# Performance work log

Measured on AMD Instinct MI355X. Metric: run time of the kernel, lower is better.

The kernel has to match this reference:

```python
import jax, jax.numpy as jnp
from jax import lax
import numpy as np

DIM = 512      # latent channel dim
K = 1024       # codebook size
KS = 320       # conv kernel size (== stride -> non-overlapping frames)
STRIDE = 320
B, L = 16, 160000  # 10s of 16kHz audio


def setup_inputs() -> dict:
    key = jax.random.key(0)
    ks = jax.random.split(key, 8)
    wav = jax.random.normal(ks[0], (B, 1, L), jnp.float32)
    enc_w = jax.random.normal(ks[1], (DIM, 1, KS), jnp.float32) * 0.05
    enc_b = jnp.zeros((DIM,), jnp.float32)
    codebook = jax.random.normal(ks[2], (K, DIM), jnp.float32)
    lin_w = jax.random.normal(ks[3], (DIM, DIM), jnp.float32) * 0.02
    lin_b = jnp.zeros((DIM,), jnp.float32)
    film_w = jax.random.normal(ks[4], (2 * DIM, DIM), jnp.float32) * 0.02
    film_b = jnp.zeros((2 * DIM,), jnp.float32)
    dec_w = jax.random.normal(ks[5], (DIM, 1, KS), jnp.float32) * 0.05
    dec_b = jnp.zeros((1,), jnp.float32)
    return dict(wav=wav, enc_w=enc_w, enc_b=enc_b, codebook=codebook,
                lin_w=lin_w, lin_b=lin_b, film_w=film_w, film_b=film_b,
                dec_w=dec_w, dec_b=dec_b)


def reference(wav, enc_w, enc_b, codebook, lin_w, lin_b, film_w, film_b, dec_w, dec_b):
    # --- NAC encoder: strided Conv1d, wav [B,1,L] -> emb [B,D,T] ---
    emb = lax.conv_general_dilated(
        wav, enc_w, window_strides=(STRIDE,), padding='VALID',
        dimension_numbers=('NCH', 'OIH', 'NCH')) + enc_b[None, :, None]

    # --- time-averaged embedding for conditioning ---
    time_avg = emb.mean(axis=-1)  # [B, D]

    # --- VQ encode: nearest codebook entry per frame ---
    x = emb.transpose(0, 2, 1)  # [B, T, D]
    # squared L2 distances [B, T, K]
    dist = (x * x).sum(-1, keepdims=True) \
         - 2.0 * jnp.einsum('btd,kd->btk', x, codebook) \
         + (codebook * codebook).sum(-1)
    codes = jnp.argmin(dist, axis=-1)  # [B, T] int

    # --- VQ decode: codebook gather ---
    emb_r = codebook[codes].transpose(0, 2, 1)  # [B, D, T]

    # --- linear on pooled embedding ---
    cond = time_avg @ lin_w.T + lin_b  # [B, D]

    # --- FiLM modulation: gamma * x + beta per channel ---
    gb = cond @ film_w.T + film_b      # [B, 2D]
    gamma, beta = jnp.split(gb, 2, axis=-1)
    modulated = gamma[:, :, None] * emb_r + beta[:, :, None]  # [B, D, T]

    # --- NAC decoder: transposed Conv1d back to waveform [B,1,L] ---
    out = lax.conv_transpose(
        modulated, dec_w, strides=(STRIDE,), padding='VALID',
        dimension_numbers=('NCH', 'IOH', 'NCH')) + dec_b[None, :, None]
    return out
```

## Files before the change

kernel.cpp:

```cpp
#include <hip/hip_runtime.h>

#define FR   8000
#define FRP  8192
#define DD   512
#define CK   1024
#define KSZ  320
#define TT   500
#define NB   16

typedef unsigned int u32;
typedef unsigned short u16;
typedef __attribute__((ext_vector_type(8))) short b8;
typedef __attribute__((ext_vector_type(4))) float f4;

__device__ __forceinline__ float bf2f(u16 h) {
    u32 u = ((u32)h) << 16;
    return __builtin_bit_cast(float, u);
}
__device__ __forceinline__ u16 f2bf(float f) {
    u32 u = __builtin_bit_cast(u32, f);
    u32 r = u + 0x7FFFu + ((u >> 16) & 1u);
    return (u16)(r >> 16);
}

__device__ __forceinline__ void gld16(const u16* g, u16* s) {
    __builtin_amdgcn_global_load_lds(
        (const __attribute__((address_space(1))) u32*)g,
        (__attribute__((address_space(3))) u32*)s, 16, 0, 0);
}

__device__ __forceinline__ f4 mfma(b8 a, b8 b, f4 c) {
    return __builtin_amdgcn_mfma_f32_16x16x32_bf16(a, b, c, 0, 0, 0);
}

__device__ __forceinline__ void split8(float4 a, float4 b, u16* dh, u16* dl) {
    float xs[8] = {a.x, a.y, a.z, a.w, b.x, b.y, b.z, b.w};
    union { u16 u[8]; b8 v; } H, L;
#pragma unroll
    for (int i = 0; i < 8; ++i) {
        u16 h = f2bf(xs[i]);
        H.u[i] = h;
        L.u[i] = f2bf(xs[i] - bf2f(h));
    }
    *(b8*)dh = H.v;
    *(b8*)dl = L.v;
}

__global__ __launch_bounds__(256) void k_prep(const float* __restrict__ enc_w,
                                              u16* __restrict__ ewh, u16* __restrict__ ewl,
                                              const float* __restrict__ cb,
                                              u16* __restrict__ cbh, u16* __restrict__ cbl,
                                              const float* __restrict__ dw,
                                              u16* __restrict__ dwfh, u16* __restrict__ dwfl,
                                              float* __restrict__ cbn,
                                              const float* __restrict__ wav,
                                              u16* __restrict__ wavh, u16* __restrict__ wavl) {
    const int bid = blockIdx.x, tid = threadIdx.x;
    if (bid < 80) {
        int i = (bid * 256 + tid) * 8;
        float4 a = *(const float4*)&enc_w[i];
        float4 b = *(const float4*)&enc_w[i + 4];
        split8(a, b, &ewh[i], &ewl[i]);
    } else if (bid < 336) {
        int i = ((bid - 80) * 256 + tid) * 8;
        float4 a = *(const float4*)&cb[i];
        float4 b = *(const float4*)&cb[i + 4];
        split8(a, b, &cbh[i], &cbl[i]);
    } else if (bid < 1104) {
        int idx = (bid - 336) * 256 + tid;
        int s = idx >> 9, d = idx & 511;
        float v = (s < KSZ) ? dw[d * KSZ + (KSZ - 1) - s] : 0.f;
        u16 hi = f2bf(v);
        dwfh[idx] = hi;
        dwfl[idx] = f2bf(v - bf2f(hi));
    } else if (bid < 1136) {
        int c = (bid - 1104) * 32 + (tid >> 3);
        int l = tid & 7;
        float s = 0.f;
        for (int j = l * 4; j < DD; j += 32) {
            float4 v = *(const float4*)&cb[c * DD + j];
            s += v.x * v.x + v.y * v.y + v.z * v.z + v.w * v.w;
        }
        s += __shfl_xor(s, 1);
        s += __shfl_xor(s, 2);
        s += __shfl_xor(s, 4);
        if (l == 0) cbn[c] = s;
    } else {
        int i = ((bid - 1136) * 256 + tid) * 8;
        float4 a = *(const float4*)&wav[i];
        float4 b = *(const float4*)&wav[i + 4];
        split8(a, b, &wavh[i], &wavl[i]);
    }
}

#define PIPELINE(NT, STRIDE)                                                  \
    stg(0, 0);                                                                \
    stg(1, STRIDE);                                                           \
    int cur = 0;                                                              \
    for (int t = 0; t < NT; ++t) {                                            \
        if (t < NT - 1) asm volatile("s_waitcnt vmcnt(8)" ::: "memory");      \
        else            asm volatile("s_waitcnt vmcnt(0)" ::: "memory");      \
        __builtin_amdgcn_s_barrier();                                         \
        asm volatile("" ::: "memory");                                        \
        compute(cur);                                                         \
        asm volatile("" ::: "memory");                                        \
        __builtin_amdgcn_s_barrier();                                         \
        if (t < NT - 2) stg(cur, (t + 2) * STRIDE);                           \
        cur ^= 1;                                                             \
    }

__global__ __launch_bounds__(256, 2) void k_enc(const u16* __restrict__ Ahg,
                                                const u16* __restrict__ Alg,
                                                const u16* __restrict__ Bhg,
                                                const u16* __restrict__ Blg,
                                                const float* __restrict__ eb,
                                                u16* __restrict__ embh,
                                                u16* __restrict__ embl) {
    __shared__ __align__(16) u16 Ah[2][4096], Al[2][4096], Bh[2][4096], Bl[2][4096];
    const int tid = threadIdx.x;
    const int l = tid & 63, w = tid >> 6, wm = w >> 1, wn = w & 1;
    const int lane16 = l & 15, laneK = l >> 4;
    const int g = blockIdx.x;
    const int xcd = g & 7, slot = g >> 3;
    const int f0 = (xcd * 8 + (slot & 7)) * 128;
    const int d0 = (slot >> 3) * 128;

    const int p0 = w * 128 + l, p1 = p0 + 64;
    const int r0 = p0 >> 2, q0 = (p0 & 3) ^ ((r0 >> 1) & 3);
    const int r1 = p1 >> 2, q1 = (p1 & 3) ^ ((r1 >> 1) & 3);
    int fa0 = f0 + r0; if (fa0 > FR - 1) fa0 = FR - 1;
    int fa1 = f0 + r1; if (fa1 > FR - 1) fa1 = FR - 1;
    const u16* gA0h = Ahg + (size_t)fa0 * KSZ + q0 * 8;
    const u16* gA1h = Ahg + (size_t)fa1 * KSZ + q1 * 8;
    const u16* gA0l = Alg + (size_t)fa0 * KSZ + q0 * 8;
    const u16* gA1l = Alg + (size_t)fa1 * KSZ + q1 * 8;
    const u16* gB0h = Bhg + (size_t)(d0 + r0) * KSZ + q0 * 8;
    const u16* gB1h = Bhg + (size_t)(d0 + r1) * KSZ + q1 * 8;
    const u16* gB0l = Blg + (size_t)(d0 + r0) * KSZ + q0 * 8;
    const u16* gB1l = Blg + (size_t)(d0 + r1) * KSZ + q1 * 8;

    int offA[4], offB[4];
#pragma unroll
    for (int i = 0; i < 4; ++i) {
        int ra = wm * 64 + i * 16 + lane16;
        offA[i] = (ra * 4 + (laneK ^ ((ra >> 1) & 3))) * 8;
        int rb = wn * 64 + i * 16 + lane16;
        offB[i] = (rb * 4 + (laneK ^ ((rb >> 1) & 3))) * 8;
    }

    f4 zero = {0.f, 0.f, 0.f, 0.f};
    f4 acc[4][4];
#pragma unroll
    for (int i = 0; i < 4; ++i)
#pragma unroll
        for (int j = 0; j < 4; ++j) acc[i][j] = zero;

    auto stg = [&](int buf, int kt) {
        gld16(gA0h + kt, Ah[buf] + w * 1024);
        gld16(gA1h + kt, Ah[buf] + w * 1024 + 512);
        gld16(gA0l + kt, Al[buf] + w * 1024);
        gld16(gA1l + kt, Al[buf] + w * 1024 + 512);
        gld16(gB0h + kt, Bh[buf] + w * 1024);
        gld16(gB1h + kt, Bh[buf] + w * 1024 + 512);
        gld16(gB0l + kt, Bl[buf] + w * 1024);
        gld16(gB1l + kt, Bl[buf] + w * 1024 + 512);
    };
    auto compute = [&](int buf) {
        b8 ah[4], al[4], bh[4], bl[4];
#pragma unroll
        for (int i = 0; i < 4; ++i) {
            ah[i] = *(const b8*)(Ah[buf] + offA[i]);
            al[i] = *(const b8*)(Al[buf] + offA[i]);
            bh[i] = *(const b8*)(Bh[buf] + offB[i]);
            bl[i] = *(const b8*)(Bl[buf] + offB[i]);
        }
#pragma unroll
        for (int mi = 0; mi < 4; ++mi)
#pragma unroll
            for (int ni = 0; ni < 4; ++ni) {
                acc[mi][ni] = mfma(ah[mi], bh[ni], acc[mi][ni]);
                acc[mi][ni] = mfma(ah[mi], bl[ni], acc[mi][ni]);
                acc[mi][ni] = mfma(al[mi], bh[ni], acc[mi][ni]);
            }
    };

    PIPELINE(10, 32)

    float ebv[4];
#pragma unroll
    for (int ni = 0; ni < 4; ++ni) ebv[ni] = eb[d0 + wn * 64 + ni * 16 + lane16];
#pragma unroll
    for (int mi = 0; mi < 4; ++mi)
#pragma unroll
        for (int q = 0; q < 4; ++q) {
            int f = f0 + wm * 64 + mi * 16 + laneK * 4 + q;
#pragma unroll
            for (int ni = 0; ni < 4; ++ni) {
                int d = d0 + wn * 64 + ni * 16 + lane16;
                float v = acc[mi][ni][q] + ebv[ni];
                u16 h = f2bf(v);
                size_t o = (size_t)f * DD + d;
                embh[o] = h;
                embl[o] = f2bf(v - bf2f(h));
            }
        }
}

__global__ __launch_bounds__(256) void k_tavg(const u16* __restrict__ eh,
                                              const u16* __restrict__ el,
                                              float* __restrict__ tavg) {
    const int b = blockIdx.y, d0 = blockIdx.x * 64;
    const int dt = threadIdx.x & 7, tg = threadIdx.x >> 3;
    const int d = d0 + dt * 8;
    float s[8] = {};
    for (int t = tg; t < TT; t += 32) {
        size_t o = (size_t)(b * TT + t) * DD + d;
        b8 h = *(const b8*)(eh + o);
        b8 lo = *(const b8*)(el + o);
#pragma unroll
        for (int j = 0; j < 8; ++j) s[j] += bf2f((u16)h[j]) + bf2f((u16)lo[j]);
    }
#pragma unroll
    for (int m = 8; m <= 32; m <<= 1)
#pragma unroll
        for (int j = 0; j < 8; ++j) s[j] += __shfl_xor(s[j], m);
    __shared__ float red[4][64];
    const int w = threadIdx.x >> 6;
    if ((threadIdx.x & 63) < 8)
#pragma unroll
        for (int j = 0; j < 8; ++j) red[w][dt * 8 + j] = s[j];
    __syncthreads();
    if (threadIdx.x < 64)
        tavg[b * DD + d0 + threadIdx.x] =
            (red[0][threadIdx.x] + red[1][threadIdx.x] +
             red[2][threadIdx.x] + red[3][threadIdx.x]) * (1.0f / TT);
}

__global__ __launch_bounds__(256) void k_cond(const float* __restrict__ tavg,
                                              const float* __restrict__ lw,
                                              const float* __restrict__ lb,
                                              float* __restrict__ cond) {
    __shared__ float stv[NB * DD];
    for (int i = threadIdx.x * 4; i < NB * DD; i += 1024)
        *(float4*)&stv[i] = *(const float4*)&tavg[i];
    __syncthreads();
    const int w = threadIdx.x >> 6, lane = threadIdx.x & 63;
    const int row = blockIdx.x * 4 + w;
    float wv[8];
#pragma unroll
    for (int j = 0; j < 8; ++j) wv[j] = lw[(size_t)row * DD + lane + 64 * j];
    float r[NB];
#pragma unroll
    for (int b = 0; b < NB; ++b) {
        float s = 0.f;
#pragma unroll
        for (int j = 0; j < 8; ++j) s += wv[j] * stv[b * DD + lane + 64 * j];
        r[b] = s;
    }
#pragma unroll
    for (int m = 32; m >= 1; m >>= 1)
#pragma unroll
        for (int b = 0; b < NB; ++b) r[b] += __shfl_xor(r[b], m);
    if (lane < NB) cond[lane * DD + row] = r[lane] + lb[row];
}

__global__ __launch_bounds__(256) void k_film(const float* __restrict__ cond,
                                              const float* __restrict__ fw,
                                              const float* __restrict__ fb,
                                              float* __restrict__ gbv) {
    __shared__ float sc[NB * DD];
    for (int i = threadIdx.x * 4; i < NB * DD; i += 1024)
        *(float4*)&sc[i] = *(const float4*)&cond[i];
    __syncthreads();
    const int w = threadIdx.x >> 6, lane = threadIdx.x & 63;
    const int row = blockIdx.x * 4 + w;
    float wv[8];
#pragma unroll
    for (int j = 0; j < 8; ++j) wv[j] = fw[(size_t)row * DD + lane + 64 * j];
    float r[NB];
#pragma unroll
    for (int b = 0; b < NB; ++b) {
        float s = 0.f;
#pragma unroll
        for (int j = 0; j < 8; ++j) s += wv[j] * sc[b * DD + lane + 64 * j];
        r[b] = s;
    }
#pragma unroll
    for (int m = 32; m >= 1; m >>= 1)
#pragma unroll
        for (int b = 0; b < NB; ++b) r[b] += __shfl_xor(r[b], m);
    if (lane < NB) gbv[lane * 2 * DD + row] = r[lane] + fb[row];
}

__global__ __launch_bounds__(256, 2) void k_dist(const u16* __restrict__ Ahg,
                                                 const u16* __restrict__ Alg,
                                                 const u16* __restrict__ Bhg,
                                                 const u16* __restrict__ Blg,
                                                 const float* __restrict__ cbn,
                                                 float* __restrict__ pmin,
                                                 int* __restrict__ pidx) {
    __shared__ __align__(16) u16 Ah[2][4096], Al[2][4096], Bh[2][4096], Bl[2][4096];
    __shared__ float s_best[128][2];
    __shared__ int s_bidx[128][2];
    const int tid = threadIdx.x;
    const int l = tid & 63, w = tid >> 6, wm = w >> 1, wn = w & 1;
    const int lane16 = l & 15, laneK = l >> 4;
    const int g = blockIdx.x;
    const int xcd = g & 7, slot = g >> 3;
    const int f0 = (xcd * 8 + (slot & 7)) * 128;
    const int c0 = (slot >> 3) * 128;
    const int cy = slot >> 3;

    const int p0 = w * 128 + l, p1 = p0 + 64;
    const int r0 = p0 >> 2, q0 = (p0 & 3) ^ ((r0 >> 1) & 3);
    const int r1 = p1 >> 2, q1 = (p1 & 3) ^ ((r1 >> 1) & 3);
    const u16* gA0h = Ahg + (size_t)(f0 + r0) * DD + q0 * 8;
    const u16* gA1h = Ahg + (size_t)(f0 + r1) * DD + q1 * 8;
    const u16* gA0l = Alg + (size_t)(f0 + r0) * DD + q0 * 8;
    const u16* gA1l = Alg + (size_t)(f0 + r1) * DD + q1 * 8;
    const u16* gB0h = Bhg + (size_t)(c0 + r0) * DD + q0 * 8;
    const u16* gB1h = Bhg + (size_t)(c0 + r1) * DD + q1 * 8;
    const u16* gB0l = Blg + (size_t)(c0 + r0) * DD + q0 * 8;
    const u16* gB1l = Blg + (size_t)(c0 + r1) * DD + q1 * 8;

    int offA[4], offB[4];
#pragma unroll
    for (int i = 0; i < 4; ++i) {
        int ra = wm * 64 + i * 16 + lane16;
        offA[i] = (ra * 4 + (laneK ^ ((ra >> 1) & 3))) * 8;
        int rb = wn * 64 + i * 16 + lane16;
        offB[i] = (rb * 4 + (laneK ^ ((rb >> 1) & 3))) * 8;
    }

    f4 zero = {0.f, 0.f, 0.f, 0.f};
    f4 acc[4][4];
#pragma unroll
    for (int i = 0; i < 4; ++i)
#pragma unroll
        for (int j = 0; j < 4; ++j) acc[i][j] = zero;

    auto stg = [&](int buf, int kt) {
        gld16(gA0h + kt, Ah[buf] + w * 1024);
        gld16(gA1h + kt, Ah[buf] + w * 1024 + 512);
        gld16(gA0l + kt, Al[buf] + w * 1024);
        gld16(gA1l + kt, Al[buf] + w * 1024 + 512);
        gld16(gB0h + kt, Bh[buf] + w * 1024);
        gld16(gB1h + kt, Bh[buf] + w * 1024 + 512);
        gld16(gB0l + kt, Bl[buf] + w * 1024);
        gld16(gB1l + kt, Bl[buf] + w * 1024 + 512);
    };
    auto compute = [&](int buf) {
        b8 ah[4], al[4], bh[4], bl[4];
#pragma unroll
        for (int i = 0; i < 4; ++i) {
            ah[i] = *(const b8*)(Ah[buf] + offA[i]);
            al[i] = *(const b8*)(Al[buf] + offA[i]);
            bh[i] = *(const b8*)(Bh[buf] + offB[i]);
            bl[i] = *(const b8*)(Bl[buf] + offB[i]);
        }
#pragma unroll
        for (int mi = 0; mi < 4; ++mi)
#pragma unroll
            for (int ni = 0; ni < 4; ++ni) {
                acc[mi][ni] = mfma(ah[mi], bh[ni], acc[mi][ni]);
                acc[mi][ni] = mfma(ah[mi], bl[ni], acc[mi][ni]);
                acc[mi][ni] = mfma(al[mi], bh[ni], acc[mi][ni]);
            }
    };

    PIPELINE(16, 32)

    float cbv[4];
    int cidx[4];
#pragma unroll
    for (int ni = 0; ni < 4; ++ni) {
        cidx[ni] = c0 + wn * 64 + ni * 16 + lane16;
        cbv[ni] = cbn[cidx[ni]];
    }
#pragma unroll
    for (int mi = 0; mi < 4; ++mi)
#pragma unroll
        for (int q = 0; q < 4; ++q) {
            float best = 3.4e38f;
            int bi = 0x7fffffff;
#pragma unroll
            for (int ni = 0; ni < 4; ++ni) {
                float s = cbv[ni] - 2.0f * acc[mi][ni][q];
                if (s < best || (s == best && cidx[ni] < bi)) { best = s; bi = cidx[ni]; }
            }
#pragma unroll
            for (int m = 8; m >= 1; m >>= 1) {
                float os = __shfl_xor(best, m);
                int oi = __shfl_xor(bi, m);
                if (os < best || (os == best && oi < bi)) { best = os; bi = oi; }
            }
            if (lane16 == 0) {
                int rl = wm * 64 + mi * 16 + laneK * 4 + q;
                s_best[rl][wn] = best;
                s_bidx[rl][wn] = bi;
            }
        }
    __syncthreads();
    if (tid < 128) {
        float b0 = s_best[tid][0], b1 = s_best[tid][1];
        int i0 = s_bidx[tid][0], i1 = s_bidx[tid][1];
        bool t1 = (b1 < b0) || (b1 == b0 && i1 < i0);
        int f = f0 + tid;
        if (f < FR) {
            pmin[f * 8 + cy] = t1 ? b1 : b0;
            pidx[f * 8 + cy] = t1 ? i1 : i0;
        }
    }
}

__global__ __launch_bounds__(256) void k_mod(const float* __restrict__ pmin,
                                             const int* __restrict__ pidx,
                                             const float* __restrict__ cb,
                                             const float* __restrict__ gbv,
                                             u16* __restrict__ mh,
                                             u16* __restrict__ ml) {
    int idx = blockIdx.x * 256 + threadIdx.x;
    int f = idx >> 6, d = (idx & 63) * 8;
    int lane = threadIdx.x & 63;
    int code = 0;
    if (lane == 0) {
        float best = pmin[f * 8];
        code = pidx[f * 8];
#pragma unroll
        for (int y = 1; y < 8; ++y) {
            float s = pmin[f * 8 + y];
            if (s < best) { best = s; code = pidx[f * 8 + y]; }
        }
    }
    code = __shfl(code, 0);
    int b = f / TT;
    const float* cp = cb + (size_t)code * DD + d;
    const float* gp = gbv + b * 2 * DD + d;
    const float* bp = gp + DD;
    union { u16 u[8]; b8 v; } H, L;
#pragma unroll
    for (int i = 0; i < 8; ++i) {
        float m = gp[i] * cp[i] + bp[i];
        u16 h = f2bf(m);
        H.u[i] = h;
        L.u[i] = f2bf(m - bf2f(h));
    }
    size_t o = (size_t)f * DD + d;
    *(b8*)&mh[o] = H.v;
    *(b8*)&ml[o] = L.v;
}

__global__ __launch_bounds__(256, 2) void k_dec(const u16* __restrict__ Ahg,
                                                const u16* __restrict__ Alg,
                                                const u16* __restrict__ Bhg,
                                                const u16* __restrict__ Blg,
                                                const float* __restrict__ db,
                                                float* __restrict__ out) {
    __shared__ __align__(16) u16 Ah[2][4096], Al[2][4096], Bh[2][4096], Bl[2][4096];
    const int tid = threadIdx.x;
    const int l = tid & 63, w = tid >> 6, wm = w >> 1, wn = w & 1;
    const int lane16 = l & 15, laneK = l >> 4;
    const int f0 = blockIdx.y * 128, s0 = blockIdx.x * 128;

    const int p0 = w * 128 + l, p1 = p0 + 64;
    const int r0 = p0 >> 2, q0 = (p0 & 3) ^ ((r0 >> 1) & 3);
    const int r1 = p1 >> 2, q1 = (p1 & 3) ^ ((r1 >> 1) & 3);
    const u16* gA0h = Ahg + (size_t)(f0 + r0) * DD + q0 * 8;
    const u16* gA1h = Ahg + (size_t)(f0 + r1) * DD + q1 * 8;
    const u16* gA0l = Alg + (size_t)(f0 + r0) * DD + q0 * 8;
    const u16* gA1l = Alg + (size_t)(f0 + r1) * DD + q1 * 8;
    const u16* gB0h = Bhg + (size_t)(s0 + r0) * DD + q0 * 8;
    const u16* gB1h = Bhg + (size_t)(s0 + r1) * DD + q1 * 8;
    const u16* gB0l = Blg + (size_t)(s0 + r0) * DD + q0 * 8;
    const u16* gB1l = Blg + (size_t)(s0 + r1) * DD + q1 * 8;

    int offA[4], offB[4];
#pragma unroll
    for (int i = 0; i < 4; ++i) {
        int ra = wm * 64 + i * 16 + lane16;
        offA[i] = (ra * 4 + (laneK ^ ((ra >> 1) & 3))) * 8;
        int rb = wn * 64 + i * 16 + lane16;
        offB[i] = (rb * 4 + (laneK ^ ((rb >> 1) & 3))) * 8;
    }

    f4 zero = {0.f, 0.f, 0.f, 0.f};
    f4 acc[4][4];
#pragma unroll
    for (int i = 0; i < 4; ++i)
#pragma unroll
        for (int j = 0; j < 4; ++j) acc[i][j] = zero;

    auto stg = [&](int buf, int kt) {
        gld16(gA0h + kt, Ah[buf] + w * 1024);
        gld16(gA1h + kt, Ah[buf] + w * 1024 + 512);
        gld16(gA0l + kt, Al[buf] + w * 1024);
        gld16(gA1l + kt, Al[buf] + w * 1024 + 512);
        gld16(gB0h + kt, Bh[buf] + w * 1024);
        gld16(gB1h + kt, Bh[buf] + w * 1024 + 512);
        gld16(gB0l + kt, Bl[buf] + w * 1024);
        gld16(gB1l + kt, Bl[buf] + w * 1024 + 512);
    };
    auto compute = [&](int buf) {
        b8 ah[4], al[4], bh[4], bl[4];
#pragma unroll
        for (int i = 0; i < 4; ++i) {
            ah[i] = *(const b8*)(Ah[buf] + offA[i]);
            al[i] = *(const b8*)(Al[buf] + offA[i]);
            bh[i] = *(const b8*)(Bh[buf] + offB[i]);
            bl[i] = *(const b8*)(Bl[buf] + offB[i]);
        }
#pragma unroll
        for (int mi = 0; mi < 4; ++mi)
#pragma unroll
            for (int ni = 0; ni < 4; ++ni) {
                acc[mi][ni] = mfma(ah[mi], bh[ni], acc[mi][ni]);
                acc[mi][ni] = mfma(ah[mi], bl[ni], acc[mi][ni]);
                acc[mi][ni] = mfma(al[mi], bh[ni], acc[mi][ni]);
            }
    };

    PIPELINE(16, 32)

    const float d0v = db[0];
#pragma unroll
    for (int mi = 0; mi < 4; ++mi)
#pragma unroll
        for (int q = 0; q < 4; ++q) {
            int f = f0 + wm * 64 + mi * 16 + laneK * 4 + q;
            if (f < FR) {
#pragma unroll
                for (int ni = 0; ni < 4; ++ni) {
                    int s = s0 + wn * 64 + ni * 16 + lane16;
                    if (s < KSZ) out[(size_t)f * KSZ + s] = acc[mi][ni][q] + d0v;
                }
            }
        }
}

extern "C" void kernel_launch(void* const* d_in, const int* in_sizes, int n_in,
                              void* d_out, int out_size, void* d_ws, size_t ws_size,
                              hipStream_t stream) {
    const float* wav    = (const float*)d_in[0];
    const float* enc_w  = (const float*)d_in[1];
    const float* enc_b  = (const float*)d_in[2];
    const float* cb     = (const float*)d_in[3];
    const float* lin_w  = (const float*)d_in[4];
    const float* lin_b  = (const float*)d_in[5];
    const float* film_w = (const float*)d_in[6];
    const float* film_b = (const float*)d_in[7];
    const float* dec_w  = (const float*)d_in[8];
    const float* dec_b  = (const float*)d_in[9];
    float* out = (float*)d_out;

    char* p = (char*)d_ws;
    u16* embh = (u16*)p;                 p += (size_t)FRP * DD * 2;
    u16* embl = (u16*)p;                 p += (size_t)FRP * DD * 2;
    u16* wavh = (u16*)p;                 p += (size_t)FR * KSZ * 2;
    u16* wavl = (u16*)p;                 p += (size_t)FR * KSZ * 2;
    u16* ewh  = (u16*)p;                 p += (size_t)DD * KSZ * 2;
    u16* ewl  = (u16*)p;                 p += (size_t)DD * KSZ * 2;
    u16* cbh  = (u16*)p;                 p += (size_t)CK * DD * 2;
    u16* cbl  = (u16*)p;                 p += (size_t)CK * DD * 2;
    u16* dwfh = (u16*)p;                 p += (size_t)384 * DD * 2;
    u16* dwfl = (u16*)p;                 p += (size_t)384 * DD * 2;
    float* cbn  = (float*)p;             p += CK * 4;
    float* tavg = (float*)p;             p += NB * DD * 4;
    float* cond = (float*)p;             p += NB * DD * 4;
    float* gbv  = (float*)p;             p += NB * 2 * DD * 4;
    float* pmin = (float*)p;             p += FR * 8 * 4;
    int*   pidx = (int*)p;               p += FR * 8 * 4;
    u16* modh = embh;
    u16* modl = embl;

    k_prep<<<dim3(2386), 256, 0, stream>>>(enc_w, ewh, ewl, cb, cbh, cbl,
                                           dec_w, dwfh, dwfl, cbn, wav, wavh, wavl);
    k_enc<<<dim3(256), 256, 0, stream>>>(wavh, wavl, ewh, ewl, enc_b, embh, embl);
    k_tavg<<<dim3(8, NB), 256, 0, stream>>>(embh, embl, tavg);
    k_cond<<<dim3(128), 256, 0, stream>>>(tavg, lin_w, lin_b, cond);
    k_film<<<dim3(256), 256, 0, stream>>>(cond, film_w, film_b, gbv);
    k_dist<<<dim3(512), 256, 0, stream>>>(embh, embl, cbh, cbl, cbn, pmin, pidx);
    k_mod<<<dim3(2000), 256, 0, stream>>>(pmin, pidx, cb, gbv, modh, modl);
    k_dec<<<dim3(3, 63), 256, 0, stream>>>(modh, modl, dwfh, dwfl, dec_b, out);
}
```

Baseline: 188.1 us.

## Fuse codebook gather and FiLM modulation into decoder GEMM; transpose dec_w via LDS

Removes the separate k_mod kernel. The decoder GEMM now resolves the argmin code per frame itself, gathers codebook rows, applies gamma/beta and splits the result to bf16 hi/lo directly into shared memory as its A operand. This drops a full round trip of the modulated hi/lo tensors through global memory and one launch. The cost is that the A tile is recomputed for each of the 3 column blocks, and the pipeline now waits with vmcnt(0) every step, giving up some load/compute overlap. Separately, the decoder-weight flip/transpose in k_prep now goes through an LDS tile so its reads and writes are coalesced.

```diff
diff --git a/kernel.cpp b/kernel.cpp
--- a/kernel.cpp
+++ b/kernel.cpp
@@ -66,15 +66,8 @@
         float4 a = *(const float4*)&cb[i];
         float4 b = *(const float4*)&cb[i + 4];
         split8(a, b, &cbh[i], &cbl[i]);
-    } else if (bid < 1104) {
-        int idx = (bid - 336) * 256 + tid;
-        int s = idx >> 9, d = idx & 511;
-        float v = (s < KSZ) ? dw[d * KSZ + (KSZ - 1) - s] : 0.f;
-        u16 hi = f2bf(v);
-        dwfh[idx] = hi;
-        dwfl[idx] = f2bf(v - bf2f(hi));
-    } else if (bid < 1136) {
-        int c = (bid - 1104) * 32 + (tid >> 3);
+    } else if (bid < 368) {
+        int c = (bid - 336) * 32 + (tid >> 3);
         int l = tid & 7;
         float s = 0.f;
         for (int j = l * 4; j < DD; j += 32) {
@@ -85,11 +78,54 @@
         s += __shfl_xor(s, 2);
         s += __shfl_xor(s, 4);
         if (l == 0) cbn[c] = s;
-    } else {
-        int i = ((bid - 1136) * 256 + tid) * 8;
+    } else if (bid < 1618) {
+        int i = ((bid - 368) * 256 + tid) * 8;
         float4 a = *(const float4*)&wav[i];
         float4 b = *(const float4*)&wav[i + 4];
         split8(a, b, &wavh[i], &wavl[i]);
+    } else {
+        int bid2 = bid - 1618;
+        int d0 = (bid2 & 7) * 64;
+        int sb = bid2 >> 3;
+        int s0 = sb * 64;
+        if (sb == 5) {
+            b8 z = {};
+#pragma unroll
+            for (int k = 0; k < 2; ++k) {
+                int lin = tid * 2 + k;
+                int row = 320 + (lin >> 3);
+                int col = (lin & 7) * 8;
+                *(b8*)&dwfh[(size_t)row * DD + d0 + col] = z;
+                *(b8*)&dwfl[(size_t)row * DD + d0 + col] = z;
+            }
+            return;
+        }
+        __shared__ float t64[64][68];
+        const int u0 = 256 - s0;
+#pragma unroll
+        for (int p = 0; p < 4; ++p) {
+            int row = (tid >> 4) + 16 * p;
+            int c4 = (tid & 15) * 4;
+            float4 v = *(const float4*)&dw[(size_t)(d0 + row) * KSZ + u0 + c4];
+            t64[row][c4] = v.x; t64[row][c4 + 1] = v.y;
+            t64[row][c4 + 2] = v.z; t64[row][c4 + 3] = v.w;
+        }
+        __syncthreads();
+        const int i = tid >> 2;
+        const int jq = (tid & 3) * 16;
+        union { u16 u[8]; b8 v; } H0, L0, H1, L1;
+#pragma unroll
+        for (int j = 0; j < 8; ++j) {
+            float m = t64[jq + j][63 - i];
+            u16 h = f2bf(m);
+            H0.u[j] = h; L0.u[j] = f2bf(m - bf2f(h));
+            float m2 = t64[jq + 8 + j][63 - i];
+            u16 h2 = f2bf(m2);
+            H1.u[j] = h2; L1.u[j] = f2bf(m2 - bf2f(h2));
+        }
+        size_t o = (size_t)(s0 + i) * DD + d0 + jq;
+        *(b8*)&dwfh[o] = H0.v; *(b8*)&dwfh[o + 8] = H1.v;
+        *(b8*)&dwfl[o] = L0.v; *(b8*)&dwfl[o + 8] = L1.v;
     }
 }
 
@@ -308,8 +344,8 @@
     const int g = blockIdx.x;
     const int xcd = g & 7, slot = g >> 3;
     const int f0 = (xcd * 8 + (slot & 7)) * 128;
-    const int c0 = (slot >> 3) * 128;
     const int cy = slot >> 3;
+    const int c0 = cy * 128;
 
     const int p0 = w * 128 + l, p1 = p0 + 64;
     const int r0 = p0 >> 2, q0 = (p0 & 3) ^ ((r0 >> 1) & 3);
@@ -413,66 +449,52 @@
     }
 }
 
-__global__ __launch_bounds__(256) void k_mod(const float* __restrict__ pmin,
-                                             const int* __restrict__ pidx,
-                                             const float* __restrict__ cb,
-                                             const float* __restrict__ gbv,
-                                             u16* __restrict__ mh,
-                                             u16* __restrict__ ml) {
-    int idx = blockIdx.x * 256 + threadIdx.x;
-    int f = idx >> 6, d = (idx & 63) * 8;
-    int lane = threadIdx.x & 63;
-    int code = 0;
-    if (lane == 0) {
-        float best = pmin[f * 8];
-        code = pidx[f * 8];
-#pragma unroll
-        for (int y = 1; y < 8; ++y) {
-            float s = pmin[f * 8 + y];
-            if (s < best) { best = s; code = pidx[f * 8 + y]; }
-        }
-    }
-    code = __shfl(code, 0);
-    int b = f / TT;
-    const float* cp = cb + (size_t)code * DD + d;
-    const float* gp = gbv + b * 2 * DD + d;
-    const float* bp = gp + DD;
-    union { u16 u[8]; b8 v; } H, L;
-#pragma unroll
-    for (int i = 0; i < 8; ++i) {
-        float m = gp[i] * cp[i] + bp[i];
-        u16 h = f2bf(m);
-        H.u[i] = h;
-        L.u[i] = f2bf(m - bf2f(h));
-    }
-    size_t o = (size_t)f * DD + d;
-    *(b8*)&mh[o] = H.v;
-    *(b8*)&ml[o] = L.v;
-}
-
-__global__ __launch_bounds__(256, 2) void k_dec(const u16* __restrict__ Ahg,
-                                                const u16* __restrict__ Alg,
+__global__ __launch_bounds__(256, 2) void k_dec(const float* __restrict__ pmin,
+                                                const int* __restrict__ pidx,
+                                                const float* __restrict__ cb,
+                                                const float* __restrict__ gbv,
                                                 const u16* __restrict__ Bhg,
                                                 const u16* __restrict__ Blg,
                                                 const float* __restrict__ db,
                                                 float* __restrict__ out) {
     __shared__ __align__(16) u16 Ah[2][4096], Al[2][4096], Bh[2][4096], Bl[2][4096];
+    __shared__ int codes_lds[128];
+    __shared__ int b_lds[128];
     const int tid = threadIdx.x;
     const int l = tid & 63, w = tid >> 6, wm = w >> 1, wn = w & 1;
     const int lane16 = l & 15, laneK = l >> 4;
     const int f0 = blockIdx.y * 128, s0 = blockIdx.x * 128;
 
+    if (tid < 128) {
+        int f = f0 + tid;
+        int fc = (f < FR) ? f : FR - 1;
+        float best = pmin[fc * 8];
+        int bi = pidx[fc * 8];
+#pragma unroll
+        for (int y = 1; y < 8; ++y) {
+            float s = pmin[fc * 8 + y];
+            if (s < best) { best = s; bi = pidx[fc * 8 + y]; }
+        }
+        codes_lds[tid] = bi;
+        b_lds[tid] = fc / TT;
+    }
+    __syncthreads();
+
     const int p0 = w * 128 + l, p1 = p0 + 64;
     const int r0 = p0 >> 2, q0 = (p0 & 3) ^ ((r0 >> 1) & 3);
     const int r1 = p1 >> 2, q1 = (p1 & 3) ^ ((r1 >> 1) & 3);
-    const u16* gA0h = Ahg + (size_t)(f0 + r0) * DD + q0 * 8;
-    const u16* gA1h = Ahg + (size_t)(f0 + r1) * DD + q1 * 8;
-    const u16* gA0l = Alg + (size_t)(f0 + r0) * DD + q0 * 8;
-    const u16* gA1l = Alg + (size_t)(f0 + r1) * DD + q1 * 8;
     const u16* gB0h = Bhg + (size_t)(s0 + r0) * DD + q0 * 8;
     const u16* gB1h = Bhg + (size_t)(s0 + r1) * DD + q1 * 8;
     const u16* gB0l = Blg + (size_t)(s0 + r0) * DD + q0 * 8;
     const u16* gB1l = Blg + (size_t)(s0 + r1) * DD + q1 * 8;
+
+    const int pa0 = tid, pa1 = tid + 256;
+    const int ra0 = pa0 >> 2, qa0 = (pa0 & 3) ^ ((ra0 >> 1) & 3);
+    const int ra1 = pa1 >> 2, qa1 = (pa1 & 3) ^ ((ra1 >> 1) & 3);
+    const float* cp0 = cb + (size_t)codes_lds[ra0] * DD + qa0 * 8;
+    const float* cp1 = cb + (size_t)codes_lds[ra1] * DD + qa1 * 8;
+    const float* gp0 = gbv + b_lds[ra0] * 2 * DD + qa0 * 8;
+    const float* gp1 = gbv + b_lds[ra1] * 2 * DD + qa1 * 8;
 
     int offA[4], offB[4];
 #pragma unroll
@@ -490,16 +512,37 @@
 #pragma unroll
         for (int j = 0; j < 4; ++j) acc[i][j] = zero;
 
-    auto stg = [&](int buf, int kt) {
-        gld16(gA0h + kt, Ah[buf] + w * 1024);
-        gld16(gA1h + kt, Ah[buf] + w * 1024 + 512);
-        gld16(gA0l + kt, Al[buf] + w * 1024);
-        gld16(gA1l + kt, Al[buf] + w * 1024 + 512);
+    auto stgB = [&](int buf, int kt) {
         gld16(gB0h + kt, Bh[buf] + w * 1024);
         gld16(gB1h + kt, Bh[buf] + w * 1024 + 512);
         gld16(gB0l + kt, Bl[buf] + w * 1024);
         gld16(gB1l + kt, Bl[buf] + w * 1024 + 512);
     };
+    auto stageA = [&](int buf, int kt) {
+        float4 c00 = *(const float4*)(cp0 + kt);
+        float4 c01 = *(const float4*)(cp0 + kt + 4);
+        float4 g00 = *(const float4*)(gp0 + kt);
+        float4 g01 = *(const float4*)(gp0 + kt + 4);
+        float4 e00 = *(const float4*)(gp0 + DD + kt);
+        float4 e01 = *(const float4*)(gp0 + DD + kt + 4);
+        float4 c10 = *(const float4*)(cp1 + kt);
+        float4 c11 = *(const float4*)(cp1 + kt + 4);
+        float4 g10 = *(const float4*)(gp1 + kt);
+        float4 g11 = *(const float4*)(gp1 + kt + 4);
+        float4 e10 = *(const float4*)(gp1 + DD + kt);
+        float4 e11 = *(const float4*)(gp1 + DD + kt + 4);
+        float4 m00, m01, m10, m11;
+        m00.x = g00.x * c00.x + e00.x; m00.y = g00.y * c00.y + e00.y;
+        m00.z = g00.z * c00.z + e00.z; m00.w = g00.w * c00.w + e00.w;
+        m01.x = g01.x * c01.x + e01.x; m01.y = g01.y * c01.y + e01.y;
+        m01.z = g01.z * c01.z + e01.z; m01.w = g01.w * c01.w + e01.w;
+        m10.x = g10.x * c10.x + e10.x; m10.y = g10.y * c10.y + e10.y;
+        m10.z = g10.z * c10.z + e10.z; m10.w = g10.w * c10.w + e10.w;
+        m11.x = g11.x * c11.x + e11.x; m11.y = g11.y * c11.y + e11.y;
+        m11.z = g11.z * c11.z + e11.z; m11.w = g11.w * c11.w + e11.w;
+        split8(m00, m01, Ah[buf] + pa0 * 8, Al[buf] + pa0 * 8);
+        split8(m10, m11, Ah[buf] + pa1 * 8, Al[buf] + pa1 * 8);
+    };
     auto compute = [&](int buf) {
         b8 ah[4], al[4], bh[4], bl[4];
 #pragma unroll
@@ -519,7 +562,19 @@
             }
     };
 
-    PIPELINE(16, 32)
+    stgB(0, 0); stageA(0, 0);
+    stgB(1, 32); stageA(1, 32);
+    int cur = 0;
+    for (int t = 0; t < 16; ++t) {
+        asm volatile("s_waitcnt vmcnt(0) lgkmcnt(0)" ::: "memory");
+        __builtin_amdgcn_s_barrier();
+        asm volatile("" ::: "memory");
+        compute(cur);
+        asm volatile("" ::: "memory");
+        __builtin_amdgcn_s_barrier();
+        if (t < 14) { stgB(cur, (t + 2) * 32); stageA(cur, (t + 2) * 32); }
+        cur ^= 1;
+    }
 
     const float d0v = db[0];
 #pragma unroll
@@ -569,16 +624,13 @@
     float* gbv  = (float*)p;             p += NB * 2 * DD * 4;
     float* pmin = (float*)p;             p += FR * 8 * 4;
     int*   pidx = (int*)p;               p += FR * 8 * 4;
-    u16* modh = embh;
-    u16* modl = embl;
-
-    k_prep<<<dim3(2386), 256, 0, stream>>>(enc_w, ewh, ewl, cb, cbh, cbl,
+
+    k_prep<<<dim3(1666), 256, 0, stream>>>(enc_w, ewh, ewl, cb, cbh, cbl,
                                            dec_w, dwfh, dwfl, cbn, wav, wavh, wavl);
     k_enc<<<dim3(256), 256, 0, stream>>>(wavh, wavl, ewh, ewl, enc_b, embh, embl);
     k_tavg<<<dim3(8, NB), 256, 0, stream>>>(embh, embl, tavg);
     k_cond<<<dim3(128), 256, 0, stream>>>(tavg, lin_w, lin_b, cond);
     k_film<<<dim3(256), 256, 0, stream>>>(cond, film_w, film_b, gbv);
     k_dist<<<dim3(512), 256, 0, stream>>>(embh, embl, cbh, cbl, cbn, pmin, pidx);
-    k_mod<<<dim3(2000), 256, 0, stream>>>(pmin, pidx, cb, gbv, modh, modl);
-    k_dec<<<dim3(3, 63), 256, 0, stream>>>(modh, modl, dwfh, dwfl, dec_b, out);
-}
+    k_dec<<<dim3(3, 63), 256, 0, stream>>>(pmin, pidx, cb, gbv, dwfh, dwfl, dec_b, out);
+}
```

After: 180.2 us. -4.2%, faster.
